# Kernel tuning notes

Measured on AMD Instinct MI355X. Metric: run time of the kernel, lower is better.

Reference implementation:

```python
import jax, jax.numpy as jnp
import numpy as np

# Module hyperparameters (from init_kwargs)
HID = 2048          # hidden_dim
LAT = 512           # kv_latent_dim
H = 16              # num_heads
D = HID // H        # head_dim = 128
FORGET_P = 0.1      # forget_prob
WIN = 128           # window_size
SINK = 16           # persistent_tokens
B, S = 2, 2048
NEG = -1e9


def setup_inputs() -> dict:
    key = jax.random.key(0)
    ks = jax.random.split(key, 8)
    scale = 0.02
    x = jax.random.normal(ks[0], (B, S, HID), dtype=jnp.float32)
    W_q = jax.random.normal(ks[1], (HID, HID), dtype=jnp.float32) * scale
    W_dkv = jax.random.normal(ks[2], (HID, LAT), dtype=jnp.float32) * scale
    W_uk = jax.random.normal(ks[3], (LAT, HID), dtype=jnp.float32) * scale
    W_uv = jax.random.normal(ks[4], (LAT, HID), dtype=jnp.float32) * scale
    W_o = jax.random.normal(ks[5], (HID, HID), dtype=jnp.float32) * scale
    # Bernoulli(forget_prob) per-key forget mask (1 = forget this token)
    forget_mask = jax.random.bernoulli(ks[6], FORGET_P, (B, S)).astype(jnp.int32)
    return {"x": x, "W_q": W_q, "W_dkv": W_dkv, "W_uk": W_uk,
            "W_uv": W_uv, "W_o": W_o, "forget_mask": forget_mask, "top_k": 64}


def reference(x, W_q, W_dkv, W_uk, W_uv, W_o, forget_mask, top_k):
    Bx, Sx, _ = x.shape
    # Queries; keys/values via shared compressed KV latent (MLA-style)
    q = (x @ W_q).reshape(Bx, Sx, H, D)
    c = x @ W_dkv                                   # [B, S, LAT]
    k = (c @ W_uk).reshape(Bx, Sx, H, D)
    v = (c @ W_uv).reshape(Bx, Sx, H, D)

    scores = jnp.einsum('bqhd,bkhd->bhqk', q, k) / np.float32(np.sqrt(D))

    qi = jnp.arange(Sx)[:, None]
    ki = jnp.arange(Sx)[None, :]
    causal = ki <= qi
    local = ki >= qi - (WIN - 1)
    sink = ki < SINK                  # persistent sink tokens always visible
    allow = causal & (local | sink)   # [S, S]

    # Forgetting: drop non-sink, non-self keys flagged by the forget mask
    forget = (forget_mask[:, None, None, :] == 1) \
             & (ki >= SINK)[None, None] & (ki != qi)[None, None]   # [B,1,S,S]
    keep = allow[None, None] & ~forget

    s = jnp.where(keep, scores, jnp.asarray(NEG, scores.dtype))
    # Top-k selection per query: keep only the k largest scores
    kth = jax.lax.top_k(s, top_k)[0][..., -1:]
    s = jnp.where(s >= kth, s, jnp.asarray(NEG, s.dtype))

    attn = jax.nn.softmax(s, axis=-1)
    out = jnp.einsum('bhqk,bkhd->bqhd', attn, v).reshape(Bx, Sx, HID)
    return out @ W_o
```

## Files before the change

kernel.cpp:

```cpp
#include <hip/hip_runtime.h>
#include <hip/hip_bf16.h>

typedef unsigned short u16;
typedef unsigned int u32;
typedef unsigned long long u64;
typedef __bf16 bf16x8 __attribute__((ext_vector_type(8)));
typedef float f32x4 __attribute__((ext_vector_type(4)));
typedef u16 u16x4 __attribute__((ext_vector_type(4)));
typedef u16 u16x8 __attribute__((ext_vector_type(8)));

static constexpr int BB = 2, SS = 2048, HIDC = 2048, LATC = 512, NH = 16, HD = 128;
static constexpr int MROWS = BB * SS;
static constexpr float NEGV = -1e9f;

__device__ __forceinline__ u16 f2bf(float f) {
  __hip_bfloat16 h = __float2bfloat16(f);
  return __builtin_bit_cast(u16, h);
}
__device__ __forceinline__ float bf2f(u16 u) {
  return __uint_as_float(((u32)u) << 16);
}
__device__ __forceinline__ void load_lds16(const void* g, void* l) {
  __builtin_amdgcn_global_load_lds(
      (const __attribute__((address_space(1))) void*)g,
      (__attribute__((address_space(3))) void*)l, 16, 0, 0);
}

template <int MODE>
__global__ __launch_bounds__(256, 2) void gemm_bt(
    const u16* __restrict__ A, const u16* __restrict__ Bt,
    float* __restrict__ C, u16* __restrict__ Cb, int M, int N, int K) {
  __shared__ u16 As[128 * 64];
  __shared__ u16 Bs[128 * 64];
  const int tid = threadIdx.x;
  const int lane = tid & 63;
  const int wv = tid >> 6;
  const int wr = wv >> 1, wc = wv & 1;
  const int m0 = blockIdx.x * 128, n0 = blockIdx.y * 128;

  f32x4 acc[4][4];
#pragma unroll
  for (int i = 0; i < 4; ++i)
#pragma unroll
    for (int j = 0; j < 4; ++j) acc[i][j] = (f32x4){0.f, 0.f, 0.f, 0.f};

  int srow[4], sgc[4];
#pragma unroll
  for (int j = 0; j < 4; ++j) {
    int e = j * 2048 + tid * 8;
    int row = e >> 6;
    int slot = (e >> 3) & 7;
    srow[j] = row;
    sgc[j] = (slot ^ (row & 7)) * 8;
  }

  for (int k0 = 0; k0 < K; k0 += 64) {
    __syncthreads();
#pragma unroll
    for (int j = 0; j < 4; ++j) {
      const u16* ga = A + (size_t)(m0 + srow[j]) * K + k0 + sgc[j];
      const u16* gb = Bt + (size_t)(n0 + srow[j]) * K + k0 + sgc[j];
      load_lds16(ga, &As[j * 2048 + wv * 512]);
      load_lds16(gb, &Bs[j * 2048 + wv * 512]);
    }
    asm volatile("s_waitcnt vmcnt(0)" ::: "memory");
    __syncthreads();

#pragma unroll
    for (int kk = 0; kk < 2; ++kk) {
      bf16x8 afr[4], bfr[4];
      const int kg = kk * 4 + (lane >> 4);
#pragma unroll
      for (int i = 0; i < 4; ++i) {
        int ar = wr * 64 + i * 16 + (lane & 15);
        afr[i] = *(const bf16x8*)&As[ar * 64 + ((kg ^ (ar & 7)) << 3)];
        int br = wc * 64 + i * 16 + (lane & 15);
        bfr[i] = *(const bf16x8*)&Bs[br * 64 + ((kg ^ (br & 7)) << 3)];
      }
#pragma unroll
      for (int mi = 0; mi < 4; ++mi)
#pragma unroll
        for (int ni = 0; ni < 4; ++ni)
          acc[mi][ni] = __builtin_amdgcn_mfma_f32_16x16x32_bf16(
              afr[mi], bfr[ni], acc[mi][ni], 0, 0, 0);
    }
  }

#pragma unroll
  for (int mi = 0; mi < 4; ++mi) {
#pragma unroll
    for (int ni = 0; ni < 4; ++ni) {
      const int row = m0 + wr * 64 + mi * 16 + (lane >> 4) * 4;
      const int col = n0 + wc * 64 + ni * 16 + (lane & 15);
#pragma unroll
      for (int r = 0; r < 4; ++r) {
        size_t off = (size_t)(row + r) * N + col;
        if constexpr (MODE == 0) C[off] = acc[mi][ni][r];
        if constexpr (MODE == 2) Cb[off] = f2bf(acc[mi][ni][r]);
      }
    }
  }
}

template <int TN, int MODE>
__global__ __launch_bounds__(256, 2) void gemm_split_bt(
    const u16* __restrict__ Ah, const u16* __restrict__ Al,
    const u16* __restrict__ Bth, const u16* __restrict__ Btl,
    float* __restrict__ C, u16* __restrict__ Ch, u16* __restrict__ Cl,
    int M, int N, int K) {
  constexpr int NI = TN / 32;
  __shared__ u16 Ash[128 * 64];
  __shared__ u16 Asl[128 * 64];
  __shared__ u16 Bsh[TN * 64];
  __shared__ u16 Bsl[TN * 64];
  const int tid = threadIdx.x;
  const int lane = tid & 63;
  const int wv = tid >> 6;
  const int wr = wv >> 1, wc = wv & 1;
  const int l15 = lane & 15, lhi = lane >> 4;
  const int m0 = blockIdx.x * 128, n0 = blockIdx.y * TN;

  f32x4 acc[4][NI];
#pragma unroll
  for (int i = 0; i < 4; ++i)
#pragma unroll
    for (int j = 0; j < NI; ++j) acc[i][j] = (f32x4){0.f, 0.f, 0.f, 0.f};

  int srow[4], sgc[4];
#pragma unroll
  for (int j = 0; j < 4; ++j) {
    int e = j * 2048 + tid * 8;
    int row = e >> 6;
    int slot = (e >> 3) & 7;
    srow[j] = row;
    sgc[j] = (slot ^ (row & 7)) * 8;
  }

  for (int k0 = 0; k0 < K; k0 += 64) {
    __syncthreads();
#pragma unroll
    for (int j = 0; j < 4; ++j) {
      const size_t ao = (size_t)(m0 + srow[j]) * K + k0 + sgc[j];
      load_lds16(Ah + ao, &Ash[j * 2048 + wv * 512]);
      load_lds16(Al + ao, &Asl[j * 2048 + wv * 512]);
    }
#pragma unroll
    for (int j = 0; j < NI; ++j) {
      const size_t bo = (size_t)(n0 + srow[j]) * K + k0 + sgc[j];
      load_lds16(Bth + bo, &Bsh[j * 2048 + wv * 512]);
      load_lds16(Btl + bo, &Bsl[j * 2048 + wv * 512]);
    }
    asm volatile("s_waitcnt vmcnt(0)" ::: "memory");
    __syncthreads();

#pragma unroll
    for (int kk = 0; kk < 2; ++kk) {
      const int kg = kk * 4 + lhi;
      bf16x8 afh[4], afl[4], bfh[NI], bfl[NI];
#pragma unroll
      for (int i = 0; i < 4; ++i) {
        const int ar = wr * 64 + i * 16 + l15;
        const int off = ar * 64 + ((kg ^ (ar & 7)) << 3);
        afh[i] = *(const bf16x8*)&Ash[off];
        afl[i] = *(const bf16x8*)&Asl[off];
      }
#pragma unroll
      for (int i = 0; i < NI; ++i) {
        const int br = wc * (TN / 2) + i * 16 + l15;
        const int off = br * 64 + ((kg ^ (br & 7)) << 3);
        bfh[i] = *(const bf16x8*)&Bsh[off];
        bfl[i] = *(const bf16x8*)&Bsl[off];
      }
#pragma unroll
      for (int mi = 0; mi < 4; ++mi)
#pragma unroll
        for (int ni = 0; ni < NI; ++ni) {
          acc[mi][ni] = __builtin_amdgcn_mfma_f32_16x16x32_bf16(
              afh[mi], bfh[ni], acc[mi][ni], 0, 0, 0);
          acc[mi][ni] = __builtin_amdgcn_mfma_f32_16x16x32_bf16(
              afh[mi], bfl[ni], acc[mi][ni], 0, 0, 0);
          acc[mi][ni] = __builtin_amdgcn_mfma_f32_16x16x32_bf16(
              afl[mi], bfh[ni], acc[mi][ni], 0, 0, 0);
        }
    }
  }

#pragma unroll
  for (int mi = 0; mi < 4; ++mi) {
#pragma unroll
    for (int ni = 0; ni < NI; ++ni) {
      const int row = m0 + wr * 64 + mi * 16 + lhi * 4;
      const int col = n0 + wc * (TN / 2) + ni * 16 + l15;
#pragma unroll
      for (int r = 0; r < 4; ++r) {
        const size_t off = (size_t)(row + r) * N + col;
        const float v = acc[mi][ni][r];
        if constexpr (MODE == 0) C[off] = v;
        if constexpr (MODE == 3) {
          const u16 hh = f2bf(v);
          Ch[off] = hh;
          Cl[off] = f2bf(v - bf2f(hh));
        }
      }
    }
  }
}

__global__ __launch_bounds__(1024) void transpose_split(
    const float* __restrict__ W, u16* __restrict__ Th, u16* __restrict__ Tl,
    int K, int N) {
  __shared__ float t[32][33];
  const int tx = threadIdx.x, ty = threadIdx.y;
  t[ty][tx] = W[(size_t)(blockIdx.y * 32 + ty) * N + blockIdx.x * 32 + tx];
  __syncthreads();
  const float v = t[tx][ty];
  const u16 hi = f2bf(v);
  const u16 lo = f2bf(v - bf2f(hi));
  const size_t o = (size_t)(blockIdx.x * 32 + ty) * K + blockIdx.y * 32 + tx;
  Th[o] = hi;
  Tl[o] = lo;
}

__global__ __launch_bounds__(1024) void transpose_one(
    const float* __restrict__ W, u16* __restrict__ T, int K, int N) {
  __shared__ float t[32][33];
  const int tx = threadIdx.x, ty = threadIdx.y;
  t[ty][tx] = W[(size_t)(blockIdx.y * 32 + ty) * N + blockIdx.x * 32 + tx];
  __syncthreads();
  const size_t o = (size_t)(blockIdx.x * 32 + ty) * K + blockIdx.y * 32 + tx;
  T[o] = f2bf(t[tx][ty]);
}

__global__ void split_ew(const float* __restrict__ in, u16* __restrict__ hi,
                         u16* __restrict__ lo, int n) {
  const size_t i = ((size_t)blockIdx.x * blockDim.x + threadIdx.x) * 4;
  if (i >= (size_t)n) return;
  f32x4 v = *(const f32x4*)(in + i);
  u16x4 h, l;
#pragma unroll
  for (int e = 0; e < 4; ++e) {
    float f = v[e];
    u16 hh = f2bf(f);
    h[e] = hh;
    l[e] = f2bf(f - bf2f(hh));
  }
  *(u16x4*)(hi + i) = h;
  *(u16x4*)(lo + i) = l;
}

__device__ __forceinline__ u32 fmap(float f) {
  u32 b = __float_as_uint(f);
  return (b & 0x80000000u) ? ~b : (b | 0x80000000u);
}
__device__ __forceinline__ float unfmap(u32 u) {
  return (u & 0x80000000u) ? __uint_as_float(u ^ 0x80000000u)
                           : __uint_as_float(~u);
}

__global__ __launch_bounds__(512, 2) void attn_v5(
    const u16* __restrict__ qbh, const u16* __restrict__ qbl,
    const u16* __restrict__ khi, const u16* __restrict__ klo,
    const u16* __restrict__ vt, const int* __restrict__ forget,
    const int* __restrict__ topk, u16* __restrict__ ab) {
  __shared__ u16 KP[2 * 64 * 128];
  __shared__ float St[64 * 68];
  __shared__ u16 Vb1[64 * 128];
  __shared__ int fm[256];
  u16* const Kh = KP;
  u16* const Kl = KP + 64 * 128;
  u16* const Pb = KP;
  u16* const Vt0 = (u16*)St;

  const float scale = 0.08838834764831845f;
  const int tid = threadIdx.x, lane = tid & 63, wv = tid >> 6;
  const int q0 = blockIdx.x * 64;
  const int h = blockIdx.y, b = blockIdx.z;
  const int mt = wv >> 1, nh = wv & 1;
  const int l15 = lane & 15, lhi = lane >> 4;
  const int nt = (q0 >= 256) ? 4 : (q0 / 64 + 1);
  const int KTOP = topk[0];

  auto kbase = [&](int t) {
    return (q0 >= 256) ? (t == 0 ? 0 : q0 + t * 64 - 192) : t * 64;
  };
  auto stage_k = [&](int t) {
    const int kbt = kbase(t);
#pragma unroll
    for (int p = 0; p < 2; ++p) {
      const int c = p * 512 + tid;
      const int row = c >> 4, sl = c & 15;
      const size_t src = (size_t)(b * SS + kbt + row) * HIDC + h * HD +
                         ((sl ^ (row & 7)) << 3);
      load_lds16(khi + src, Kh + (p * 512 + wv * 64) * 8);
      load_lds16(klo + src, Kl + (p * 512 + wv * 64) * 8);
    }
  };
  auto stage_vt = [&](int t, u16* dst) {
    const int kbt = kbase(t);
#pragma unroll
    for (int p = 0; p < 2; ++p) {
      const int c = p * 512 + tid;
      const int d = c >> 3, sl = c & 7;
      const u16* src = vt + ((size_t)(b * HIDC + h * HD + d)) * SS + kbt +
                       ((sl ^ (d & 7)) << 3);
      load_lds16(src, dst + (p * 512 + wv * 64) * 8);
    }
  };

  if (tid < 256)
    fm[tid] = ((tid >> 6) < nt) ? forget[b * SS + kbase(tid >> 6) + (tid & 63)] : 0;

  u16x8 ah[4], al[4];
  const size_t qrow = (size_t)(b * SS + q0 + mt * 16 + l15) * HIDC + h * HD;
#pragma unroll
  for (int kt = 0; kt < 4; ++kt) {
    ah[kt] = *(const u16x8*)(qbh + qrow + kt * 32 + lhi * 8);
    al[kt] = *(const u16x8*)(qbl + qrow + kt * 32 + lhi * 8);
  }

  u32 uu[8][4];
#pragma unroll
  for (int i = 0; i < 8; ++i)
#pragma unroll
    for (int j = 0; j < 4; ++j) uu[i][j] = 0u;

  stage_k(0);
#pragma unroll
  for (int t = 0; t < 4; ++t) {
    if (t < nt) {
      asm volatile("s_waitcnt vmcnt(0)" ::: "memory");
      __syncthreads();

      f32x4 acc0 = (f32x4){0.f, 0.f, 0.f, 0.f};
      f32x4 acc1 = (f32x4){0.f, 0.f, 0.f, 0.f};
#pragma unroll
      for (int kt = 0; kt < 4; ++kt) {
        const int kg = kt * 4 + lhi;
#pragma unroll
        for (int ni = 0; ni < 2; ++ni) {
          const int key = nh * 32 + ni * 16 + l15;
          const int off = key * 128 + ((kg ^ (key & 7)) << 3);
          const bf16x8 bh = *(const bf16x8*)(Kh + off);
          const bf16x8 bl = *(const bf16x8*)(Kl + off);
          f32x4 a = ni ? acc1 : acc0;
          a = __builtin_amdgcn_mfma_f32_16x16x32_bf16(
              __builtin_bit_cast(bf16x8, ah[kt]), bh, a, 0, 0, 0);
          a = __builtin_amdgcn_mfma_f32_16x16x32_bf16(
              __builtin_bit_cast(bf16x8, ah[kt]), bl, a, 0, 0, 0);
          a = __builtin_amdgcn_mfma_f32_16x16x32_bf16(
              __builtin_bit_cast(bf16x8, al[kt]), bh, a, 0, 0, 0);
          if (ni) acc1 = a; else acc0 = a;
        }
      }
#pragma unroll
      for (int ni = 0; ni < 2; ++ni)
#pragma unroll
        for (int r = 0; r < 4; ++r)
          St[(mt * 16 + lhi * 4 + r) * 68 + nh * 32 + ni * 16 + l15] =
              (ni ? acc1 : acc0)[r] * scale;
      __syncthreads();

      if (t + 1 < nt) stage_k(t + 1);

      const int kbt = kbase(t);
#pragma unroll
      for (int i = 0; i < 8; ++i) {
        const int qi = q0 + wv * 8 + i;
        const int key = kbt + lane;
        const bool valid =
            key <= qi && (key >= qi - 127 || key < 16) &&
            !(fm[t * 64 + lane] && key >= 16 && key != qi);
        uu[i][t] = fmap(valid ? St[(wv * 8 + i) * 68 + lane] : NEGV);
      }
    }
  }
  __syncthreads();

  stage_vt(0, Vt0);

  u32 tl[8], th[8];
#pragma unroll
  for (int i = 0; i < 8; ++i) { tl[i] = 0u; th[i] = 0xFFFFFFFFu; }
  for (int it = 0; it < 32; ++it) {
#pragma unroll
    for (int i = 0; i < 8; ++i) {
      const u32 mid = tl[i] + ((th[i] - tl[i]) >> 1) + 1u;
      const int cnt = __popcll(__ballot(uu[i][0] >= mid)) +
                      __popcll(__ballot(uu[i][1] >= mid)) +
                      __popcll(__ballot(uu[i][2] >= mid)) +
                      __popcll(__ballot(uu[i][3] >= mid));
      const bool ge = cnt >= KTOP;
      tl[i] = ge ? mid : tl[i];
      th[i] = ge ? th[i] : mid - 1u;
    }
  }

#pragma unroll
  for (int i = 0; i < 8; ++i) {
    const int r = wv * 8 + i;
    float sv[4], m = NEGV;
#pragma unroll
    for (int j = 0; j < 4; ++j) {
      sv[j] = unfmap(uu[i][j]);
      m = (uu[i][j] >= tl[i]) ? fmaxf(m, sv[j]) : m;
    }
#pragma unroll
    for (int off = 32; off > 0; off >>= 1) m = fmaxf(m, __shfl_xor(m, off));
    float e[4], z = 0.f;
#pragma unroll
    for (int j = 0; j < 4; ++j) {
      e[j] = (uu[i][j] >= tl[i]) ? __expf(sv[j] - m) : 0.f;
      z += e[j];
    }
#pragma unroll
    for (int off = 32; off > 0; off >>= 1) z += __shfl_xor(z, off);
    const float rz = 1.f / z;
#pragma unroll
    for (int j = 0; j < 4; ++j) {
      const int c = lane + 64 * j;
      const int sl = c >> 3;
      Pb[r * 256 + ((sl ^ (r & 7)) << 3) + (c & 7)] = f2bf(e[j] * rz);
    }
  }

  asm volatile("s_waitcnt vmcnt(0)" ::: "memory");
  __syncthreads();

  f32x4 pacc[4];
#pragma unroll
  for (int t2 = 0; t2 < 4; ++t2) pacc[t2] = (f32x4){0.f, 0.f, 0.f, 0.f};

#pragma unroll
  for (int t = 0; t < 4; ++t) {
    if (t < nt) {
      if (t + 1 < nt) stage_vt(t + 1, ((t + 1) & 1) ? Vb1 : Vt0);
      const u16* Vcur = (t & 1) ? Vb1 : Vt0;
#pragma unroll
      for (int ks = 0; ks < 2; ++ks) {
        const int arow = mt * 16 + l15;
        const int aslot = t * 8 + ks * 4 + lhi;
        const bf16x8 af =
            *(const bf16x8*)(Pb + arow * 256 + ((aslot ^ (arow & 7)) << 3));
#pragma unroll
        for (int t2 = 0; t2 < 4; ++t2) {
          const int drow = nh * 64 + t2 * 16 + l15;
          const int dslot = ks * 4 + lhi;
          const bf16x8 bf_ =
              *(const bf16x8*)(Vcur + drow * 64 + ((dslot ^ (drow & 7)) << 3));
          pacc[t2] = __builtin_amdgcn_mfma_f32_16x16x32_bf16(af, bf_, pacc[t2],
                                                             0, 0, 0);
        }
      }
      if (t + 1 < nt) {
        asm volatile("s_waitcnt vmcnt(0)" ::: "memory");
        __syncthreads();
      }
    }
  }

#pragma unroll
  for (int t2 = 0; t2 < 4; ++t2)
#pragma unroll
    for (int r = 0; r < 4; ++r) {
      const int row = q0 + mt * 16 + lhi * 4 + r;
      const int col = h * HD + nh * 64 + t2 * 16 + l15;
      ab[(size_t)(b * SS + row) * HIDC + col] = f2bf(pacc[t2][r]);
    }
}

extern "C" void kernel_launch(void* const* d_in, const int* in_sizes, int n_in,
                              void* d_out, int out_size, void* d_ws, size_t ws_size,
                              hipStream_t stream) {
  const float* x = (const float*)d_in[0];
  const float* W_q = (const float*)d_in[1];
  const float* W_dkv = (const float*)d_in[2];
  const float* W_uk = (const float*)d_in[3];
  const float* W_uv = (const float*)d_in[4];
  const float* W_o = (const float*)d_in[5];
  const int* forget = (const int*)d_in[6];
  const int* topk = (const int*)d_in[7];
  float* out = (float*)d_out;

  char* p = (char*)d_ws;
  auto take = [&](size_t n) {
    char* r = p;
    p += (n + 255) & ~(size_t)255;
    return r;
  };

  u16* xb_hi = (u16*)take((size_t)MROWS * HIDC * 2);
  u16* xb_lo = (u16*)take((size_t)MROWS * HIDC * 2);
  u16* Wqh = (u16*)take((size_t)HIDC * HIDC * 2);
  u16* Wql = (u16*)take((size_t)HIDC * HIDC * 2);
  u16* Wdh = (u16*)take((size_t)LATC * HIDC * 2);
  u16* Wdl = (u16*)take((size_t)LATC * HIDC * 2);
  u16* Wukh = (u16*)take((size_t)HIDC * LATC * 2);
  u16* Wukl = (u16*)take((size_t)HIDC * LATC * 2);
  u16* Wuvt = (u16*)take((size_t)HIDC * LATC * 2);
  u16* Wot = (u16*)take((size_t)HIDC * HIDC * 2);
  u16* qbh = (u16*)take((size_t)MROWS * HIDC * 2);
  u16* qbl = (u16*)take((size_t)MROWS * HIDC * 2);
  u16* cbh = (u16*)take((size_t)MROWS * LATC * 2);
  u16* cbl = (u16*)take((size_t)MROWS * LATC * 2);
  u16* vt = (u16*)take((size_t)BB * HIDC * SS * 2);
  u16* khi = xb_hi;
  u16* klo = xb_lo;
  u16* ab = Wqh;

  const dim3 tb(32, 32);
  split_ew<<<dim3((MROWS * HIDC / 4) / 256), dim3(256), 0, stream>>>(
      x, xb_hi, xb_lo, MROWS * HIDC);
  transpose_split<<<dim3(HIDC / 32, HIDC / 32), tb, 0, stream>>>(W_q, Wqh, Wql, HIDC, HIDC);
  transpose_split<<<dim3(LATC / 32, HIDC / 32), tb, 0, stream>>>(W_dkv, Wdh, Wdl, HIDC, LATC);
  transpose_split<<<dim3(HIDC / 32, LATC / 32), tb, 0, stream>>>(W_uk, Wukh, Wukl, LATC, HIDC);
  transpose_one<<<dim3(HIDC / 32, LATC / 32), tb, 0, stream>>>(W_uv, Wuvt, LATC, HIDC);
  transpose_one<<<dim3(HIDC / 32, HIDC / 32), tb, 0, stream>>>(W_o, Wot, HIDC, HIDC);

  gemm_split_bt<128, 3><<<dim3(MROWS / 128, HIDC / 128), 256, 0, stream>>>(
      xb_hi, xb_lo, Wqh, Wql, nullptr, qbh, qbl, MROWS, HIDC, HIDC);
  gemm_split_bt<64, 3><<<dim3(MROWS / 128, LATC / 64), 256, 0, stream>>>(
      xb_hi, xb_lo, Wdh, Wdl, nullptr, cbh, cbl, MROWS, LATC, HIDC);
  gemm_split_bt<128, 3><<<dim3(MROWS / 128, HIDC / 128), 256, 0, stream>>>(
      cbh, cbl, Wukh, Wukl, nullptr, khi, klo, MROWS, HIDC, LATC);
  const dim3 gv(HIDC / 128, SS / 128);
  gemm_bt<2><<<gv, 256, 0, stream>>>(Wuvt, cbh, nullptr, vt, HIDC, SS, LATC);
  gemm_bt<2><<<gv, 256, 0, stream>>>(Wuvt, cbh + (size_t)SS * LATC, nullptr,
                                     vt + (size_t)HIDC * SS, HIDC, SS, LATC);
  attn_v5<<<dim3(SS / 64, NH, BB), dim3(512), 0, stream>>>(
      qbh, qbl, khi, klo, vt, forget, topk, ab);
  gemm_bt<0><<<dim3(MROWS / 128, HIDC / 128), 256, 0, stream>>>(
      ab, Wot, out, nullptr, MROWS, HIDC, HIDC);
}
```

Before: 349.4 us.

## Remap attention blocks across XCDs, hoist LDS offsets, early-exit top-k bisection

The attention kernel remaps the linear block index so consecutive blocks land on the same XCD with neighbouring query tiles, which should improve L2 reuse of K/V. It precomputes the swizzled LDS offsets for K, P and V reads once, instead of recomputing them every loop iteration, and hoists the per-key mask terms out of the row loop. The top-k threshold bisection now stops a row once its count exactly matches k and exits the loop when every row has converged, which can skip most of the 32 iterations. The early-exit branches add divergence, and an exact-match stop still gives a valid threshold for selection.

```diff
diff --git a/kernel.cpp b/kernel.cpp
--- a/kernel.cpp
+++ b/kernel.cpp
@@ -257,7 +257,7 @@
                            : __uint_as_float(~u);
 }
 
-__global__ __launch_bounds__(512, 2) void attn_v5(
+__global__ __launch_bounds__(512, 2) void attn_v6(
     const u16* __restrict__ qbh, const u16* __restrict__ qbl,
     const u16* __restrict__ khi, const u16* __restrict__ klo,
     const u16* __restrict__ vt, const int* __restrict__ forget,
@@ -273,8 +273,11 @@
 
   const float scale = 0.08838834764831845f;
   const int tid = threadIdx.x, lane = tid & 63, wv = tid >> 6;
-  const int q0 = blockIdx.x * 64;
-  const int h = blockIdx.y, b = blockIdx.z;
+  const int lin = blockIdx.x + 32 * (blockIdx.y + 16 * blockIdx.z);
+  const int nl = (lin & 7) * 128 + (lin >> 3);
+  const int q0 = (nl & 31) * 64;
+  const int h = (nl >> 5) & 15;
+  const int b = nl >> 9;
   const int mt = wv >> 1, nh = wv & 1;
   const int l15 = lane & 15, lhi = lane >> 4;
   const int nt = (q0 >= 256) ? 4 : (q0 / 64 + 1);
@@ -310,6 +313,30 @@
   if (tid < 256)
     fm[tid] = ((tid >> 6) < nt) ? forget[b * SS + kbase(tid >> 6) + (tid & 63)] : 0;
 
+  u32 koff[4][2];
+#pragma unroll
+  for (int kt = 0; kt < 4; ++kt)
+#pragma unroll
+    for (int ni = 0; ni < 2; ++ni) {
+      const int key = nh * 32 + ni * 16 + l15;
+      const int kg = kt * 4 + lhi;
+      koff[kt][ni] = key * 128 + ((kg ^ (key & 7)) << 3);
+    }
+  const int arow = mt * 16 + l15;
+  u32 pboff[2];
+#pragma unroll
+  for (int ks = 0; ks < 2; ++ks)
+    pboff[ks] = arow * 256 + (((ks * 4 + lhi) ^ (arow & 7)) << 3);
+  u32 voff[2][4];
+#pragma unroll
+  for (int ks = 0; ks < 2; ++ks)
+#pragma unroll
+    for (int t2 = 0; t2 < 4; ++t2) {
+      const int drow = nh * 64 + t2 * 16 + l15;
+      voff[ks][t2] = drow * 64 + (((ks * 4 + lhi) ^ (drow & 7)) << 3);
+    }
+  const u32 stw = (u32)(mt * 16 + lhi * 4) * 68 + nh * 32 + l15;
+
   u16x8 ah[4], al[4];
   const size_t qrow = (size_t)(b * SS + q0 + mt * 16 + l15) * HIDC + h * HD;
 #pragma unroll
@@ -335,13 +362,10 @@
       f32x4 acc1 = (f32x4){0.f, 0.f, 0.f, 0.f};
 #pragma unroll
       for (int kt = 0; kt < 4; ++kt) {
-        const int kg = kt * 4 + lhi;
 #pragma unroll
         for (int ni = 0; ni < 2; ++ni) {
-          const int key = nh * 32 + ni * 16 + l15;
-          const int off = key * 128 + ((kg ^ (key & 7)) << 3);
-          const bf16x8 bh = *(const bf16x8*)(Kh + off);
-          const bf16x8 bl = *(const bf16x8*)(Kl + off);
+          const bf16x8 bh = *(const bf16x8*)(Kh + koff[kt][ni]);
+          const bf16x8 bl = *(const bf16x8*)(Kl + koff[kt][ni]);
           f32x4 a = ni ? acc1 : acc0;
           a = __builtin_amdgcn_mfma_f32_16x16x32_bf16(
               __builtin_bit_cast(bf16x8, ah[kt]), bh, a, 0, 0, 0);
@@ -356,20 +380,20 @@
       for (int ni = 0; ni < 2; ++ni)
 #pragma unroll
         for (int r = 0; r < 4; ++r)
-          St[(mt * 16 + lhi * 4 + r) * 68 + nh * 32 + ni * 16 + l15] =
-              (ni ? acc1 : acc0)[r] * scale;
+          St[stw + r * 68 + ni * 16] = (ni ? acc1 : acc0)[r] * scale;
       __syncthreads();
 
       if (t + 1 < nt) stage_k(t + 1);
 
       const int kbt = kbase(t);
+      const int key = kbt + lane;
+      const bool fok = !(fm[t * 64 + lane] != 0 && key >= 16);
+      const bool sk = key < 16;
 #pragma unroll
       for (int i = 0; i < 8; ++i) {
         const int qi = q0 + wv * 8 + i;
-        const int key = kbt + lane;
         const bool valid =
-            key <= qi && (key >= qi - 127 || key < 16) &&
-            !(fm[t * 64 + lane] && key >= 16 && key != qi);
+            key <= qi && (key >= qi - 127 || sk) && (fok || key == qi);
         uu[i][t] = fmap(valid ? St[(wv * 8 + i) * 68 + lane] : NEGV);
       }
     }
@@ -382,17 +406,27 @@
 #pragma unroll
   for (int i = 0; i < 8; ++i) { tl[i] = 0u; th[i] = 0xFFFFFFFFu; }
   for (int it = 0; it < 32; ++it) {
+    bool any = false;
 #pragma unroll
     for (int i = 0; i < 8; ++i) {
-      const u32 mid = tl[i] + ((th[i] - tl[i]) >> 1) + 1u;
-      const int cnt = __popcll(__ballot(uu[i][0] >= mid)) +
-                      __popcll(__ballot(uu[i][1] >= mid)) +
-                      __popcll(__ballot(uu[i][2] >= mid)) +
-                      __popcll(__ballot(uu[i][3] >= mid));
-      const bool ge = cnt >= KTOP;
-      tl[i] = ge ? mid : tl[i];
-      th[i] = ge ? th[i] : mid - 1u;
-    }
+      if (tl[i] < th[i]) {
+        any = true;
+        const u32 mid = tl[i] + ((th[i] - tl[i]) >> 1) + 1u;
+        const int cnt = __popcll(__ballot(uu[i][0] >= mid)) +
+                        __popcll(__ballot(uu[i][1] >= mid)) +
+                        __popcll(__ballot(uu[i][2] >= mid)) +
+                        __popcll(__ballot(uu[i][3] >= mid));
+        if (cnt == KTOP) {
+          tl[i] = mid;
+          th[i] = mid;
+        } else if (cnt > KTOP) {
+          tl[i] = mid;
+        } else {
+          th[i] = mid - 1u;
+        }
+      }
+    }
+    if (!any) break;
   }
 
 #pragma unroll
@@ -437,16 +471,10 @@
       const u16* Vcur = (t & 1) ? Vb1 : Vt0;
 #pragma unroll
       for (int ks = 0; ks < 2; ++ks) {
-        const int arow = mt * 16 + l15;
-        const int aslot = t * 8 + ks * 4 + lhi;
-        const bf16x8 af =
-            *(const bf16x8*)(Pb + arow * 256 + ((aslot ^ (arow & 7)) << 3));
+        const bf16x8 af = *(const bf16x8*)(Pb + pboff[ks] + t * 64);
 #pragma unroll
         for (int t2 = 0; t2 < 4; ++t2) {
-          const int drow = nh * 64 + t2 * 16 + l15;
-          const int dslot = ks * 4 + lhi;
-          const bf16x8 bf_ =
-              *(const bf16x8*)(Vcur + drow * 64 + ((dslot ^ (drow & 7)) << 3));
+          const bf16x8 bf_ = *(const bf16x8*)(Vcur + voff[ks][t2]);
           pacc[t2] = __builtin_amdgcn_mfma_f32_16x16x32_bf16(af, bf_, pacc[t2],
                                                              0, 0, 0);
         }
@@ -526,7 +554,7 @@
   gemm_bt<2><<<gv, 256, 0, stream>>>(Wuvt, cbh, nullptr, vt, HIDC, SS, LATC);
   gemm_bt<2><<<gv, 256, 0, stream>>>(Wuvt, cbh + (size_t)SS * LATC, nullptr,
                                      vt + (size_t)HIDC * SS, HIDC, SS, LATC);
-  attn_v5<<<dim3(SS / 64, NH, BB), dim3(512), 0, stream>>>(
+  attn_v6<<<dim3(SS / 64, NH, BB), dim3(512), 0, stream>>>(
       qbh, qbl, khi, klo, vt, forget, topk, ab);
   gemm_bt<0><<<dim3(MROWS / 128, HIDC / 128), 256, 0, stream>>>(
       ab, Wot, out, nullptr, MROWS, HIDC, HIDC);
```

New measurement: 330.6 us. 5.4% less time.
